# Optimization experiments

Measured on AMD Instinct MI355X. Metric: run time of the kernel, lower is better.

The kernel has to match this reference:

```python
import jax, jax.numpy as jnp
import numpy as np


def setup_inputs() -> dict:
    key = jax.random.key(0)
    ks = jax.random.split(key, 9)
    B, Lq, Lk, D = 8, 2048, 2048, 768
    s = 1.0 / np.sqrt(D)
    return {
        "queries": jax.random.normal(ks[0], (B, Lq, D), dtype=jnp.float32),
        "values": jax.random.normal(ks[1], (B, Lk, D), dtype=jnp.float32),
        "mask": jax.random.randint(ks[2], (B, Lq, Lk), 0, 2) > 0,
        "Wq": jax.random.normal(ks[3], (D, D), dtype=jnp.float32) * s,
        "bq": jax.random.normal(ks[4], (D,), dtype=jnp.float32) * s,
        "Wk": jax.random.normal(ks[5], (D, D), dtype=jnp.float32) * s,
        "bk": jax.random.normal(ks[6], (D,), dtype=jnp.float32) * s,
        "Wv": jax.random.normal(ks[7], (D, D), dtype=jnp.float32) * s,
        "bv": jax.random.normal(ks[8], (D,), dtype=jnp.float32) * s,
    }


def reference(queries, values, mask, Wq, bq, Wk, bk, Wv, bv):
    NEG = jnp.asarray(-1e9, queries.dtype)
    # torch Linear: x @ W.T + b
    q = jnp.einsum("bld,ed->ble", queries, Wq) + bq
    v = jnp.einsum("bld,ed->ble", values, Wv) + bv
    # NOTE (faithful to source): keys are the key-projection of the
    # already value-projected tensor.
    k = jnp.einsum("bld,ed->ble", v, Wk) + bk
    score = jnp.einsum("bqd,bkd->bqk", q, k)  # [B, Lq, Lk]
    score = jnp.where(mask, score, NEG)
    attn = jax.nn.sigmoid(score)  # sigmoid attention, no normalization
    context = jnp.einsum("bqk,bkd->bqd", attn, v)
    return context
```

## Files before the change

kernel.cpp:

```cpp
#include <hip/hip_runtime.h>
#include <hip/hip_bf16.h>

typedef __bf16 bf16_t;
typedef __bf16 bf16x8 __attribute__((ext_vector_type(8)));
typedef __bf16 bf16x4 __attribute__((ext_vector_type(4)));
typedef float  f32x4  __attribute__((ext_vector_type(4)));

#define LDS_DST(p) ((__attribute__((address_space(3))) void*)(p))
#define GLB_SRC(p) ((const __attribute__((address_space(1))) void*)(p))

#define SBAR()   asm volatile("s_barrier" ::: "memory")
#define WVM8()   asm volatile("s_waitcnt vmcnt(8)" ::: "memory")
#define WVM4()   asm volatile("s_waitcnt vmcnt(4)" ::: "memory")
#define WVM0()   asm volatile("s_waitcnt vmcnt(0)" ::: "memory")
#define SP1()    __builtin_amdgcn_s_setprio(1)
#define SP0()    __builtin_amdgcn_s_setprio(0)

__global__ void __launch_bounds__(256)
prep_kernel(const int* __restrict__ mask, unsigned long long* __restrict__ bits,
            const float* __restrict__ q_in, const float* __restrict__ v_in,
            const float* __restrict__ wq_in, const float* __restrict__ wk_in,
            const float* __restrict__ wv_in,
            bf16_t* __restrict__ qb, bf16_t* __restrict__ vb,
            bf16_t* __restrict__ wqb, bf16_t* __restrict__ wkb,
            bf16_t* __restrict__ wvb) {
  const int bid = blockIdx.x;
  const int tid = threadIdx.x;
  if (bid < 16384) {
    const long wid = (((long)bid * 256 + tid) >> 6);
    const int lane = tid & 63;
    const long base = wid * 512;
    unsigned long long b[8];
#pragma unroll
    for (int i = 0; i < 8; ++i)
      b[i] = __ballot(mask[base + i * 64 + lane] != 0);
    if (lane == 0) {
      unsigned long long* o = bits + wid * 8;
#pragma unroll
      for (int i = 0; i < 8; ++i) o[i] = b[i];
    }
    return;
  }
  const float* in; bf16_t* out; int i;
  int r = bid - 16384;
  if (r < 24576) {
    in = (r < 12288) ? q_in : v_in;
    out = (r < 12288) ? qb : vb;
    i = (r % 12288) * 256 + tid;
  } else {
    r -= 24576;
    in = (r < 576) ? wq_in : (r < 1152 ? wk_in : wv_in);
    out = (r < 576) ? wqb : (r < 1152 ? wkb : wvb);
    i = (r % 576) * 256 + tid;
    if (i >= 147456) return;
  }
  const float4 v = reinterpret_cast<const float4*>(in)[i];
  bf16x4 o;
  o[0] = (bf16_t)v.x; o[1] = (bf16_t)v.y; o[2] = (bf16_t)v.z; o[3] = (bf16_t)v.w;
  reinterpret_cast<bf16x4*>(out)[i] = o;
}

__global__ void __launch_bounds__(256)
transpose_bf16_kernel(const bf16_t* __restrict__ in, bf16_t* __restrict__ out,
                      int R, int C) {
  __shared__ bf16_t tile[64][72];
  const long base = (long)blockIdx.z * R * C;
  const bf16_t* ib = in + base;
  bf16_t* ob = out + base;
  const int r0 = blockIdx.x * 64, c0 = blockIdx.y * 64;
  const int tid = threadIdx.x;
  const int rr = tid >> 3, cg = tid & 7;
#pragma unroll
  for (int p = 0; p < 2; ++p) {
    int row = p * 32 + rr;
    bf16x8 v = *reinterpret_cast<const bf16x8*>(ib + (long)(r0 + row) * C + c0 + cg * 8);
    *reinterpret_cast<bf16x8*>(&tile[row][cg * 8]) = v;
  }
  __syncthreads();
#pragma unroll
  for (int p = 0; p < 2; ++p) {
    int c = p * 32 + rr;
    bf16x8 v;
#pragma unroll
    for (int i = 0; i < 8; ++i) v[i] = tile[cg * 8 + i][c];
    *reinterpret_cast<bf16x8*>(ob + (long)(c0 + c) * R + r0 + cg * 8) = v;
  }
}


__device__ __forceinline__ void read_A(const char* smem, int off, bf16x8 (&af)[8], int xk0) {
#pragma unroll
  for (int mf = 0; mf < 4; ++mf)
#pragma unroll
    for (int kk = 0; kk < 2; ++kk)
      af[mf * 2 + kk] = *reinterpret_cast<const bf16x8*>(
          smem + off + mf * 2048 + (kk ? (xk0 ^ 64) : xk0));
}

__device__ __forceinline__ void read_B(const char* smem, int off, bf16x8 (&bf_)[4], int xk0) {
#pragma unroll
  for (int nf = 0; nf < 2; ++nf)
#pragma unroll
    for (int kk = 0; kk < 2; ++kk)
      bf_[nf * 2 + kk] = *reinterpret_cast<const bf16x8*>(
          smem + off + nf * 2048 + (kk ? (xk0 ^ 64) : xk0));
}

template <int MH, int NH>
__device__ __forceinline__ void mfma_q(const bf16x8 (&af)[8], const bf16x8 (&bf_)[4],
                                       f32x4 (&acc)[8][4]) {
#pragma unroll
  for (int mf = 0; mf < 4; ++mf)
#pragma unroll
    for (int nf = 0; nf < 2; ++nf)
#pragma unroll
      for (int kk = 0; kk < 2; ++kk)
        acc[MH * 4 + mf][NH * 2 + nf] = __builtin_amdgcn_mfma_f32_16x16x32_bf16(
            af[mf * 2 + kk], bf_[nf * 2 + kk], acc[MH * 4 + mf][NH * 2 + nf], 0, 0, 0);
}

#define STAGE_A(slot, mh, kt) do {                                            \
  _Pragma("unroll") for (int j_ = 0; j_ < 2; ++j_)                            \
    __builtin_amdgcn_global_load_lds(                                         \
        GLB_SRC(pA + (long)(j_ * 128 + (mh) * 64) * K + (kt)),                \
        LDS_DST(smem + (slot) * 65536 + (arow0 + j_ * 128 + (mh) * 64) * 128),\
        16, 0, 0);                                                            \
} while (0)

#define STAGE_B(slot, nh, kt) do {                                            \
  _Pragma("unroll") for (int j_ = 0; j_ < 2; ++j_)                            \
    __builtin_amdgcn_global_load_lds(                                         \
        GLB_SRC(pB + (long)(j_ * 128 + (nh) * 32) * K + (kt)),                \
        LDS_DST(smem + (slot) * 65536 + 32768 +                               \
                (brow0 + j_ * 128 + (nh) * 32) * 128),                        \
        16, 0, 0);                                                            \
} while (0)

template <int MODE>
__global__ void __launch_bounds__(512, 2)
gemm8p_kernel(const bf16_t* __restrict__ A, const bf16_t* __restrict__ B,
              const float* __restrict__ bias, const unsigned* __restrict__ maskbits,
              void* __restrict__ Cout, int M, int N, int K,
              long sA, long sB, long sC, long sMask,
              const bf16_t* __restrict__ A2, const bf16_t* __restrict__ B2,
              const float* __restrict__ bias2, void* __restrict__ C2) {
  __shared__ __align__(1024) char smem[131072];

  const int gx = gridDim.x, gy = gridDim.y;
  int f0 = blockIdx.x + gx * (blockIdx.y + gy * blockIdx.z);
  const int nwg = gx * gy * (int)gridDim.z;
  const int q8 = nwg >> 3, r8 = nwg & 7;
  const int xcd = f0 & 7, idx = f0 >> 3;
  int f1 = (xcd < r8 ? xcd * (q8 + 1) : r8 * (q8 + 1) + (xcd - r8) * q8) + idx;
  int bxi, byi, bz;
  if constexpr (MODE == 1) {
    bxi = f1 & 7;
    const int byL = (f1 >> 3) & 1;
    const int st = (f1 >> 4) & 3;
    bz = f1 >> 6;
    byi = st * 2 + byL;
  } else {
    byi = f1 % gy;
    const int t = f1 / gy;
    bxi = t % gx;
    bz = t / gx;
  }

  const bf16_t* Ab; const bf16_t* Bb;
  const float* biasp = bias; void* Cp = Cout;
  if constexpr (MODE == 0) {
    if (bz) { Ab = A2; Bb = B2; biasp = bias2; Cp = C2; }
    else    { Ab = A;  Bb = B; }
  } else {
    Ab = A + bz * sA; Bb = B + bz * sB;
  }
  const int bm = bxi * 256, bn = byi * 256;
  const int tid = threadIdx.x;
  const int wave = tid >> 6, lane = tid & 63;
  const int wr = wave >> 2, wc = wave & 3;
  const int l15 = lane & 15, lg = lane >> 4;
  const int xk0 = (lg * 16) ^ ((lane & 7) << 4);
  const int NT = K >> 6;

  const int lr = lane >> 3;
  const int cgs = ((lane & 7) ^ lr) * 8;
  const int arow0 = wave * 8;
  const int brow0 = (wave >> 2) * 64 + (wave & 3) * 8;
  const bf16_t* pA = Ab + (long)(bm + arow0 + lr) * K + cgs;
  const bf16_t* pB = Bb + (long)(bn + brow0 + lr) * K + cgs;

  const int aoff = wr * 16384 + l15 * 128;
  const int boff = 32768 + wc * 8192 + l15 * 128;

  f32x4 acc[8][4] = {};
  bf16x8 afX[8], bfB[4], bf0[4];

  STAGE_A(0, 0, 0); STAGE_B(0, 0, 0); STAGE_B(0, 1, 0); STAGE_A(0, 1, 0);
  STAGE_A(1, 0, 64); STAGE_B(1, 0, 64);
  STAGE_B(1, 1, 64); STAGE_A(1, 1, 64);
  WVM8();
  SBAR();
  read_A(smem, aoff + 0, afX, xk0);
  read_B(smem, boff + 0, bf0, xk0);

  int slot = 0;
  for (int t = 0; t + 2 < NT; ++t) {
    const int so = slot * 65536, sn = (slot ^ 1) * 65536;
    const int k2 = (t + 2) << 6;
    read_B(smem, so + boff + 4096, bfB, xk0);
    STAGE_A(slot, 0, k2); STAGE_B(slot, 0, k2);
    SP1(); mfma_q<0, 0>(afX, bf0, acc); SP0();
    SP1(); mfma_q<0, 1>(afX, bfB, acc); SP0();
    read_A(smem, so + aoff + 8192, afX, xk0);
    WVM8(); SBAR();
    SP1(); mfma_q<1, 1>(afX, bfB, acc); SP0();
    SP1(); mfma_q<1, 0>(afX, bf0, acc); SP0();
    read_A(smem, sn + aoff + 0, afX, xk0);
    read_B(smem, sn + boff + 0, bf0, xk0);
    STAGE_B(slot, 1, k2); STAGE_A(slot, 1, k2);
    WVM8(); SBAR();
    slot ^= 1;
  }

  {
    const int so = slot * 65536, sn = (slot ^ 1) * 65536;
    read_B(smem, so + boff + 4096, bfB, xk0);
    SP1(); mfma_q<0, 0>(afX, bf0, acc); SP0();
    SP1(); mfma_q<0, 1>(afX, bfB, acc); SP0();
    read_A(smem, so + aoff + 8192, afX, xk0);
    WVM4(); SBAR();
    SP1(); mfma_q<1, 1>(afX, bfB, acc); SP0();
    SP1(); mfma_q<1, 0>(afX, bf0, acc); SP0();
    read_A(smem, sn + aoff + 0, afX, xk0);
    read_B(smem, sn + boff + 0, bf0, xk0);
    WVM0(); SBAR();
    read_B(smem, sn + boff + 4096, bfB, xk0);
    SP1(); mfma_q<0, 0>(afX, bf0, acc); SP0();
    SP1(); mfma_q<0, 1>(afX, bfB, acc); SP0();
    read_A(smem, sn + aoff + 8192, afX, xk0);
    SP1(); mfma_q<1, 1>(afX, bfB, acc); SP0();
    SP1(); mfma_q<1, 0>(afX, bf0, acc); SP0();
  }

  float* eb = (float*)smem;
  const int lrow = tid >> 3, t7 = tid & 7;
#pragma unroll
  for (int rd = 0; rd < 4; ++rd) {
    __syncthreads();
#pragma unroll
    for (int fi = 0; fi < 2; ++fi)
#pragma unroll
      for (int nf = 0; nf < 4; ++nf)
#pragma unroll
        for (int r = 0; r < 4; ++r) {
          const int lr2 = wr * 32 + fi * 16 + lg * 4 + r;
          eb[lr2 * 256 + wc * 64 + nf * 16 + l15] = acc[rd * 2 + fi][nf][r];
        }
    __syncthreads();
    const int growt = rd * 32 + lrow + ((lrow >> 5) * 96);
    const long rowbase = (long)(bm + growt) * N + bn;
    if constexpr (MODE == 1) {
      const unsigned* mw =
          maskbits + bz * sMask + (long)(bm + growt) * (N >> 5) + (bn >> 5);
      const uint4 w0 = *reinterpret_cast<const uint4*>(mw);
      const uint4 w1 = *reinterpret_cast<const uint4*>(mw + 4);
      const unsigned wq[8] = {w0.x, w0.y, w0.z, w0.w, w1.x, w1.y, w1.z, w1.w};
#pragma unroll
      for (int q = 0; q < 8; ++q) {
        const int c4 = (q * 8 + t7) * 4;
        const f32x4 v = *reinterpret_cast<const f32x4*>(&eb[lrow * 256 + c4]);
        const unsigned nib = (wq[q] >> (t7 * 4)) & 0xFu;
        bf16x4 o;
        o[0] = (bf16_t)((nib & 1u) ? __builtin_amdgcn_rcpf(1.f + __expf(-v[0])) : 0.f);
        o[1] = (bf16_t)((nib & 2u) ? __builtin_amdgcn_rcpf(1.f + __expf(-v[1])) : 0.f);
        o[2] = (bf16_t)((nib & 4u) ? __builtin_amdgcn_rcpf(1.f + __expf(-v[2])) : 0.f);
        o[3] = (bf16_t)((nib & 8u) ? __builtin_amdgcn_rcpf(1.f + __expf(-v[3])) : 0.f);
        *reinterpret_cast<bf16x4*>((bf16_t*)Cp + bz * sC + rowbase + c4) = o;
      }
    } else {
#pragma unroll
      for (int q = 0; q < 8; ++q) {
        const int c4 = (q * 8 + t7) * 4;
        const f32x4 v = *reinterpret_cast<const f32x4*>(&eb[lrow * 256 + c4]);
        if constexpr (MODE == 0) {
          const f32x4 b4 = *reinterpret_cast<const f32x4*>(biasp + bn + c4);
          bf16x4 o;
          o[0] = (bf16_t)(v[0] + b4[0]); o[1] = (bf16_t)(v[1] + b4[1]);
          o[2] = (bf16_t)(v[2] + b4[2]); o[3] = (bf16_t)(v[3] + b4[3]);
          *reinterpret_cast<bf16x4*>((bf16_t*)Cp + bz * sC + rowbase + c4) = o;
        } else {
          *reinterpret_cast<f32x4*>((float*)Cp + bz * sC + rowbase + c4) = v;
        }
      }
    }
  }
}

extern "C" void kernel_launch(void* const* d_in, const int* in_sizes, int n_in,
                              void* d_out, int out_size, void* d_ws, size_t ws_size,
                              hipStream_t stream) {
  const float* queries = (const float*)d_in[0];
  const float* values  = (const float*)d_in[1];
  const int*   mask    = (const int*)d_in[2];
  const float* Wq = (const float*)d_in[3];
  const float* bq = (const float*)d_in[4];
  const float* Wk = (const float*)d_in[5];
  const float* bk = (const float*)d_in[6];
  const float* Wv = (const float*)d_in[7];
  const float* bv = (const float*)d_in[8];

  char* ws = (char*)d_ws;
  bf16_t* qb  = (bf16_t*)(ws + 0);
  bf16_t* vb  = (bf16_t*)(ws + 25165824);
  bf16_t* wqb = (bf16_t*)(ws + 50331648);
  bf16_t* wkb = (bf16_t*)(ws + 51511296);
  bf16_t* wvb = (bf16_t*)(ws + 52690944);
  bf16_t* qp  = (bf16_t*)(ws + 53870592);
  bf16_t* vp  = (bf16_t*)(ws + 79036416);
  bf16_t* kp  = (bf16_t*)(ws + 104202240);
  bf16_t* vpT = (bf16_t*)(ws + 129368064);
  bf16_t* P   = (bf16_t*)(ws + 154533888);
  unsigned long long* mbits = (unsigned long long*)(ws + 221642752);

  prep_kernel<<<42688, 256, 0, stream>>>(mask, mbits, queries, values,
                                         Wq, Wk, Wv, qb, vb, wqb, wkb, wvb);

  const dim3 blk2(512);

  gemm8p_kernel<0><<<dim3(64, 3, 2), blk2, 0, stream>>>(
      qb, wqb, bq, nullptr, qp, 16384, 768, 768, 0, 0, 0, 0,
      vb, wvb, bv, vp);
  gemm8p_kernel<0><<<dim3(64, 3, 1), blk2, 0, stream>>>(
      vp, wkb, bk, nullptr, kp, 16384, 768, 768, 0, 0, 0, 0,
      vp, wkb, bk, kp);

  transpose_bf16_kernel<<<dim3(32, 12, 8), 256, 0, stream>>>(vp, vpT, 2048, 768);

  gemm8p_kernel<1><<<dim3(8, 8, 8), blk2, 0, stream>>>(
      qp, kp, nullptr, (const unsigned*)mbits, P, 2048, 2048, 768,
      (long)2048 * 768, (long)2048 * 768, (long)2048 * 2048, (long)2048 * 64,
      nullptr, nullptr, nullptr, nullptr);

  gemm8p_kernel<2><<<dim3(8, 3, 8), blk2, 0, stream>>>(
      P, vpT, nullptr, nullptr, d_out, 2048, 768, 2048,
      (long)2048 * 2048, (long)768 * 2048, (long)2048 * 768, 0,
      nullptr, nullptr, nullptr, nullptr);
}
```

Measured before the change: 262.7 us.

## Fuse mask reading into score GEMM epilogue and drop mask bit-packing pass

Removes the separate pass that packed the int32 mask into bitmasks, leaving a plain fp32-to-bf16 convert kernel. The score GEMM epilogue now reads the raw int mask directly, issuing the int4 loads before the LDS staging barrier so their latency overlaps the accumulator write-out. This avoids one full-grid pass over the 128MB mask plus the bitmask write and read. In exchange, the GEMM epilogue becomes heavily memory-bound, and the 32 extra registers held for mask values raise pressure under the 512x2 launch bounds.

```diff
diff --git a/kernel.cpp b/kernel.cpp
--- a/kernel.cpp
+++ b/kernel.cpp
@@ -17,32 +17,15 @@
 #define SP0()    __builtin_amdgcn_s_setprio(0)
 
 __global__ void __launch_bounds__(256)
-prep_kernel(const int* __restrict__ mask, unsigned long long* __restrict__ bits,
-            const float* __restrict__ q_in, const float* __restrict__ v_in,
-            const float* __restrict__ wq_in, const float* __restrict__ wk_in,
-            const float* __restrict__ wv_in,
-            bf16_t* __restrict__ qb, bf16_t* __restrict__ vb,
-            bf16_t* __restrict__ wqb, bf16_t* __restrict__ wkb,
-            bf16_t* __restrict__ wvb) {
-  const int bid = blockIdx.x;
+convert_kernel(const float* __restrict__ q_in, const float* __restrict__ v_in,
+               const float* __restrict__ wq_in, const float* __restrict__ wk_in,
+               const float* __restrict__ wv_in,
+               bf16_t* __restrict__ qb, bf16_t* __restrict__ vb,
+               bf16_t* __restrict__ wqb, bf16_t* __restrict__ wkb,
+               bf16_t* __restrict__ wvb) {
   const int tid = threadIdx.x;
-  if (bid < 16384) {
-    const long wid = (((long)bid * 256 + tid) >> 6);
-    const int lane = tid & 63;
-    const long base = wid * 512;
-    unsigned long long b[8];
-#pragma unroll
-    for (int i = 0; i < 8; ++i)
-      b[i] = __ballot(mask[base + i * 64 + lane] != 0);
-    if (lane == 0) {
-      unsigned long long* o = bits + wid * 8;
-#pragma unroll
-      for (int i = 0; i < 8; ++i) o[i] = b[i];
-    }
-    return;
-  }
+  int r = blockIdx.x;
   const float* in; bf16_t* out; int i;
-  int r = bid - 16384;
   if (r < 24576) {
     in = (r < 12288) ? q_in : v_in;
     out = (r < 12288) ? qb : vb;
@@ -52,7 +35,6 @@
     in = (r < 576) ? wq_in : (r < 1152 ? wk_in : wv_in);
     out = (r < 576) ? wqb : (r < 1152 ? wkb : wvb);
     i = (r % 576) * 256 + tid;
-    if (i >= 147456) return;
   }
   const float4 v = reinterpret_cast<const float4*>(in)[i];
   bf16x4 o;
@@ -139,7 +121,7 @@
 template <int MODE>
 __global__ void __launch_bounds__(512, 2)
 gemm8p_kernel(const bf16_t* __restrict__ A, const bf16_t* __restrict__ B,
-              const float* __restrict__ bias, const unsigned* __restrict__ maskbits,
+              const float* __restrict__ bias, const int* __restrict__ mask,
               void* __restrict__ Cout, int M, int N, int K,
               long sA, long sB, long sC, long sMask,
               const bf16_t* __restrict__ A2, const bf16_t* __restrict__ B2,
@@ -246,6 +228,15 @@
   const int lrow = tid >> 3, t7 = tid & 7;
 #pragma unroll
   for (int rd = 0; rd < 4; ++rd) {
+    const int growt = rd * 32 + lrow + ((lrow >> 5) * 96);
+    const long rowbase = (long)(bm + growt) * N + bn;
+    int4 m4[8];
+    if constexpr (MODE == 1) {
+      const int* mrow = mask + bz * sMask + rowbase;
+#pragma unroll
+      for (int q = 0; q < 8; ++q)
+        m4[q] = *reinterpret_cast<const int4*>(mrow + (q * 8 + t7) * 4);
+    }
     __syncthreads();
 #pragma unroll
     for (int fi = 0; fi < 2; ++fi)
@@ -257,40 +248,25 @@
           eb[lr2 * 256 + wc * 64 + nf * 16 + l15] = acc[rd * 2 + fi][nf][r];
         }
     __syncthreads();
-    const int growt = rd * 32 + lrow + ((lrow >> 5) * 96);
-    const long rowbase = (long)(bm + growt) * N + bn;
-    if constexpr (MODE == 1) {
-      const unsigned* mw =
-          maskbits + bz * sMask + (long)(bm + growt) * (N >> 5) + (bn >> 5);
-      const uint4 w0 = *reinterpret_cast<const uint4*>(mw);
-      const uint4 w1 = *reinterpret_cast<const uint4*>(mw + 4);
-      const unsigned wq[8] = {w0.x, w0.y, w0.z, w0.w, w1.x, w1.y, w1.z, w1.w};
-#pragma unroll
-      for (int q = 0; q < 8; ++q) {
-        const int c4 = (q * 8 + t7) * 4;
-        const f32x4 v = *reinterpret_cast<const f32x4*>(&eb[lrow * 256 + c4]);
-        const unsigned nib = (wq[q] >> (t7 * 4)) & 0xFu;
+#pragma unroll
+    for (int q = 0; q < 8; ++q) {
+      const int c4 = (q * 8 + t7) * 4;
+      const f32x4 v = *reinterpret_cast<const f32x4*>(&eb[lrow * 256 + c4]);
+      if constexpr (MODE == 1) {
         bf16x4 o;
-        o[0] = (bf16_t)((nib & 1u) ? __builtin_amdgcn_rcpf(1.f + __expf(-v[0])) : 0.f);
-        o[1] = (bf16_t)((nib & 2u) ? __builtin_amdgcn_rcpf(1.f + __expf(-v[1])) : 0.f);
-        o[2] = (bf16_t)((nib & 4u) ? __builtin_amdgcn_rcpf(1.f + __expf(-v[2])) : 0.f);
-        o[3] = (bf16_t)((nib & 8u) ? __builtin_amdgcn_rcpf(1.f + __expf(-v[3])) : 0.f);
+        o[0] = (bf16_t)(m4[q].x ? __builtin_amdgcn_rcpf(1.f + __expf(-v[0])) : 0.f);
+        o[1] = (bf16_t)(m4[q].y ? __builtin_amdgcn_rcpf(1.f + __expf(-v[1])) : 0.f);
+        o[2] = (bf16_t)(m4[q].z ? __builtin_amdgcn_rcpf(1.f + __expf(-v[2])) : 0.f);
+        o[3] = (bf16_t)(m4[q].w ? __builtin_amdgcn_rcpf(1.f + __expf(-v[3])) : 0.f);
         *reinterpret_cast<bf16x4*>((bf16_t*)Cp + bz * sC + rowbase + c4) = o;
-      }
-    } else {
-#pragma unroll
-      for (int q = 0; q < 8; ++q) {
-        const int c4 = (q * 8 + t7) * 4;
-        const f32x4 v = *reinterpret_cast<const f32x4*>(&eb[lrow * 256 + c4]);
-        if constexpr (MODE == 0) {
-          const f32x4 b4 = *reinterpret_cast<const f32x4*>(biasp + bn + c4);
-          bf16x4 o;
-          o[0] = (bf16_t)(v[0] + b4[0]); o[1] = (bf16_t)(v[1] + b4[1]);
-          o[2] = (bf16_t)(v[2] + b4[2]); o[3] = (bf16_t)(v[3] + b4[3]);
-          *reinterpret_cast<bf16x4*>((bf16_t*)Cp + bz * sC + rowbase + c4) = o;
-        } else {
-          *reinterpret_cast<f32x4*>((float*)Cp + bz * sC + rowbase + c4) = v;
-        }
+      } else if constexpr (MODE == 0) {
+        const f32x4 b4 = *reinterpret_cast<const f32x4*>(biasp + bn + c4);
+        bf16x4 o;
+        o[0] = (bf16_t)(v[0] + b4[0]); o[1] = (bf16_t)(v[1] + b4[1]);
+        o[2] = (bf16_t)(v[2] + b4[2]); o[3] = (bf16_t)(v[3] + b4[3]);
+        *reinterpret_cast<bf16x4*>((bf16_t*)Cp + bz * sC + rowbase + c4) = o;
+      } else {
+        *reinterpret_cast<f32x4*>((float*)Cp + bz * sC + rowbase + c4) = v;
       }
     }
   }
@@ -320,10 +296,9 @@
   bf16_t* kp  = (bf16_t*)(ws + 104202240);
   bf16_t* vpT = (bf16_t*)(ws + 129368064);
   bf16_t* P   = (bf16_t*)(ws + 154533888);
-  unsigned long long* mbits = (unsigned long long*)(ws + 221642752);
-
-  prep_kernel<<<42688, 256, 0, stream>>>(mask, mbits, queries, values,
-                                         Wq, Wk, Wv, qb, vb, wqb, wkb, wvb);
+
+  convert_kernel<<<26304, 256, 0, stream>>>(queries, values, Wq, Wk, Wv,
+                                            qb, vb, wqb, wkb, wvb);
 
   const dim3 blk2(512);
 
@@ -337,8 +312,8 @@
   transpose_bf16_kernel<<<dim3(32, 12, 8), 256, 0, stream>>>(vp, vpT, 2048, 768);
 
   gemm8p_kernel<1><<<dim3(8, 8, 8), blk2, 0, stream>>>(
-      qp, kp, nullptr, (const unsigned*)mbits, P, 2048, 2048, 768,
-      (long)2048 * 768, (long)2048 * 768, (long)2048 * 2048, (long)2048 * 64,
+      qp, kp, nullptr, mask, P, 2048, 2048, 768,
+      (long)2048 * 768, (long)2048 * 768, (long)2048 * 2048, (long)2048 * 2048,
       nullptr, nullptr, nullptr, nullptr);
 
   gemm8p_kernel<2><<<dim3(8, 3, 8), blk2, 0, stream>>>(
```

Result: no change. 259.3 us (-1.3%).
